# Kernel optimization log

Hardware: AMD Instinct MI355X
Metric: run time of the kernel (lower is better)

The kernel has to match this reference:

```python
import jax, jax.numpy as jnp
import numpy as np

B, S, D = 2, 2048, 1024
H = 16
HD = D // H


def setup_inputs() -> dict:
    key = jax.random.key(0)
    k = jax.random.split(key, 5)
    s = 0.02
    return {
        "x": jax.random.normal(k[0], (B, S, D), jnp.float32),
        "w_qkv": jax.random.normal(k[1], (3 * D, D), jnp.float32) * s,
        "b_qkv": jax.random.normal(k[2], (3 * D,), jnp.float32) * s,
        "w_out": jax.random.normal(k[3], (D, D), jnp.float32) * s,
        "b_out": jax.random.normal(k[4], (D,), jnp.float32) * s,
    }


def reference(x, w_qkv, b_qkv, w_out, b_out):
    b, s, d = x.shape
    h, hd = H, HD
    scale = hd ** -0.5
    # QKV projection: [B,S,3D] -> [3,B,H,S,hd]
    qkv = x @ w_qkv.T + b_qkv
    qkv = qkv.reshape(b, s, 3, h, hd).transpose(2, 0, 3, 1, 4)
    q, k, v = qkv[0], qkv[1], qkv[2]
    # Attention scores [B,H,S,S]
    scores = jnp.einsum("bhqd,bhkd->bhqk", q, k) * scale
    attn = jax.nn.softmax(scores, axis=-1)
    # Attend and merge heads
    attended = jnp.einsum("bhqk,bhkd->bqhd", attn, v).reshape(b, s, d)
    return attended @ w_out.T + b_out
```

## Files before the change

### kernel.cpp

```cpp
#include <hip/hip_runtime.h>
#include <hip/hip_bf16.h>

typedef __hip_bfloat16 bf16;
typedef __attribute__((ext_vector_type(8))) short short8;
typedef __attribute__((ext_vector_type(8))) __bf16 bf16x8;
typedef __attribute__((ext_vector_type(2))) float f32x2;
typedef __attribute__((ext_vector_type(4))) float f32x4;
typedef __attribute__((ext_vector_type(16))) float f32x16;
typedef __attribute__((ext_vector_type(4))) unsigned int u32x4;
typedef __attribute__((ext_vector_type(2))) unsigned int u32x2;

#define MFMA16(a, b, c)                                                        \
  __builtin_amdgcn_mfma_f32_16x16x32_bf16(__builtin_bit_cast(bf16x8, (a)),     \
                                          __builtin_bit_cast(bf16x8, (b)),     \
                                          (c), 0, 0, 0)
#define MFMA32(a, b, c)                                                        \
  __builtin_amdgcn_mfma_f32_32x32x16_bf16(__builtin_bit_cast(bf16x8, (a)),     \
                                          __builtin_bit_cast(bf16x8, (b)),     \
                                          (c), 0, 0, 0)

#define GLD16(gsrc, ldst)                                                      \
  __builtin_amdgcn_global_load_lds(                                            \
      (const __attribute__((address_space(1))) void*)(gsrc),                   \
      (__attribute__((address_space(3))) void*)(ldst), 16, 0, 0)

__device__ inline unsigned pk2(float lo, float hi) {
  unsigned r;
  asm("v_cvt_pk_bf16_f32 %0, %1, %2" : "=v"(r) : "v"(lo), "v"(hi));
  return r;
}
__device__ inline f32x2 pkfma(f32x2 s, f32x2 m, f32x2 a) {
  f32x2 r;
  asm("v_pk_fma_f32 %0, %1, %2, %3" : "=v"(r) : "v"(s), "v"(m), "v"(a));
  return r;
}
__device__ inline short f2bfs(float f) {
  return __builtin_bit_cast(short, __float2bfloat16(f));
}

template <typename T> __device__ inline short8 ld8bf(const T* p);
template <> __device__ inline short8 ld8bf<bf16>(const bf16* p) {
  return *(const short8*)p;
}
template <> __device__ inline short8 ld8bf<float>(const float* p) {
  f32x4 a = *(const f32x4*)p;
  f32x4 b = *(const f32x4*)(p + 4);
  u32x4 r;
  r[0] = pk2(a[0], a[1]);
  r[1] = pk2(a[2], a[3]);
  r[2] = pk2(b[0], b[1]);
  r[3] = pk2(b[2], b[3]);
  return __builtin_bit_cast(short8, r);
}

template <typename OT> __device__ inline void st1(OT* p, float v);
template <> __device__ inline void st1<bf16>(bf16* p, float v) {
  *p = __float2bfloat16(v);
}
template <> __device__ inline void st1<float>(float* p, float v) { *p = v; }

__device__ inline unsigned int funnel16(unsigned int hi, unsigned int lo) {
  return (unsigned int)(((((unsigned long long)hi) << 32) | lo) >> 16);
}
__device__ inline short8 rotl8(short8 v, int r) {
  u32x4 W = __builtin_bit_cast(u32x4, v);
  u32x4 T, U, F;
  int wr = r >> 1;
  T[0] = (wr & 1) ? W[1] : W[0];
  T[1] = (wr & 1) ? W[2] : W[1];
  T[2] = (wr & 1) ? W[3] : W[2];
  T[3] = (wr & 1) ? W[0] : W[3];
  U[0] = (wr & 2) ? T[2] : T[0];
  U[1] = (wr & 2) ? T[3] : T[1];
  U[2] = (wr & 2) ? T[0] : T[2];
  U[3] = (wr & 2) ? T[1] : T[3];
  F[0] = (r & 1) ? funnel16(U[1], U[0]) : U[0];
  F[1] = (r & 1) ? funnel16(U[2], U[1]) : U[1];
  F[2] = (r & 1) ? funnel16(U[3], U[2]) : U[2];
  F[3] = (r & 1) ? funnel16(U[0], U[3]) : U[3];
  return __builtin_bit_cast(short8, F);
}

__global__ __launch_bounds__(256) void cvt3(
    const float* __restrict__ s0, bf16* __restrict__ d0, int n0,
    const float* __restrict__ s1, bf16* __restrict__ d1, int n1,
    const float* __restrict__ s2, bf16* __restrict__ d2, int n2) {
  int i = (blockIdx.x * 256 + threadIdx.x) * 8;
  if (i < n0) {
    *(short8*)&d0[i] = ld8bf(s0 + i);
  } else if ((i -= n0) < n1) {
    *(short8*)&d1[i] = ld8bf(s1 + i);
  } else if ((i -= n1) < n2) {
    *(short8*)&d2[i] = ld8bf(s2 + i);
  }
}

template <int BN, typename OT>
__global__ __launch_bounds__(256, 2) void gemm_lds_bias(
    const bf16* __restrict__ A, const bf16* __restrict__ B,
    const float* __restrict__ bias, OT* __restrict__ C, int M, int N, int K) {
  __shared__ bf16 As[128][64];
  __shared__ bf16 Bs[BN][64];

  const int tid = threadIdx.x;
  const int w = tid >> 6, l = tid & 63;
  const int wr = w >> 1, wc = w & 1;
  const int m0 = blockIdx.y * 128, n0 = blockIdx.x * BN;
  const int JN = BN / 64;
  const int WCOL = BN / 2;

  f32x4 acc[4][2 * JN] = {};

  const int srow = l >> 3;
  const int scol = (l & 7) * 8;

  for (int kt = 0; kt < K; kt += 64) {
#pragma unroll
    for (int j = 0; j < 4; ++j) {
      int chunk = w * 4 + j;
      int row = chunk * 8 + srow;
      GLD16(A + (size_t)(m0 + row) * K + kt + scol, &As[0][0] + chunk * 512);
    }
#pragma unroll
    for (int j = 0; j < BN / 32; ++j) {
      int chunk = w * (BN / 32) + j;
      int row = chunk * 8 + srow;
      GLD16(B + (size_t)(n0 + row) * K + kt + scol, &Bs[0][0] + chunk * 512);
    }
    __syncthreads();

#pragma unroll
    for (int kk = 0; kk < 2; ++kk) {
      short8 af[4], bfv[2 * JN];
#pragma unroll
      for (int i = 0; i < 4; ++i)
        af[i] = *(const short8*)&As[wr * 64 + i * 16 + (l & 15)]
                                  [kk * 32 + (l >> 4) * 8];
#pragma unroll
      for (int jn = 0; jn < 2 * JN; ++jn)
        bfv[jn] = *(const short8*)&Bs[wc * WCOL + jn * 16 + (l & 15)]
                                    [kk * 32 + (l >> 4) * 8];
#pragma unroll
      for (int i = 0; i < 4; ++i)
#pragma unroll
        for (int jn = 0; jn < 2 * JN; ++jn)
          acc[i][jn] = MFMA16(af[i], bfv[jn], acc[i][jn]);
    }
    __syncthreads();
  }

#pragma unroll
  for (int i = 0; i < 4; ++i) {
    int rbase = m0 + wr * 64 + i * 16 + (l >> 4) * 4;
#pragma unroll
    for (int jn = 0; jn < 2 * JN; ++jn) {
      int col = n0 + wc * WCOL + jn * 16 + (l & 15);
      float bv = bias[col];
#pragma unroll
      for (int r = 0; r < 4; ++r)
        st1(&C[(size_t)(rbase + r) * N + col], acc[i][jn][r] + bv);
    }
  }
}

template <typename AT, typename OT>
__global__ __launch_bounds__(256, 2) void gemm_bt_bias(
    const AT* __restrict__ A, const float* __restrict__ B,
    const float* __restrict__ bias, OT* __restrict__ C, int M, int N, int K) {
  __shared__ bf16 As[128][64];
  __shared__ bf16 Bs[128][64];

  const int tid = threadIdx.x;
  const int w = tid >> 6, l = tid & 63;
  const int wr = w >> 1, wc = w & 1;
  const int m0 = blockIdx.y * 128, n0 = blockIdx.x * 128;

  f32x4 acc[4][4] = {};

  const int srow = tid >> 3;
  const int scol = (tid & 7) * 8;

  for (int kt = 0; kt < K; kt += 64) {
    short8 aReg[4], bReg[4];
#pragma unroll
    for (int p = 0; p < 4; ++p) {
      int row = p * 32 + srow;
      aReg[p] = ld8bf(A + (size_t)(m0 + row) * K + kt + scol);
      bReg[p] = ld8bf(B + (size_t)(n0 + row) * K + kt + scol);
    }
    __syncthreads();
#pragma unroll
    for (int p = 0; p < 4; ++p) {
      int row = p * 32 + srow;
      *(short8*)&As[row][scol] = aReg[p];
      *(short8*)&Bs[row][scol] = bReg[p];
    }
    __syncthreads();

#pragma unroll
    for (int kk = 0; kk < 2; ++kk) {
      short8 af[4], bfv[4];
#pragma unroll
      for (int i = 0; i < 4; ++i) {
        af[i]  = *(const short8*)&As[wr * 64 + i * 16 + (l & 15)]
                                   [kk * 32 + (l >> 4) * 8];
        bfv[i] = *(const short8*)&Bs[wc * 64 + i * 16 + (l & 15)]
                                   [kk * 32 + (l >> 4) * 8];
      }
#pragma unroll
      for (int i = 0; i < 4; ++i)
#pragma unroll
        for (int jn = 0; jn < 4; ++jn)
          acc[i][jn] = MFMA16(af[i], bfv[jn], acc[i][jn]);
    }
  }

#pragma unroll
  for (int i = 0; i < 4; ++i) {
    int rbase = m0 + wr * 64 + i * 16 + (l >> 4) * 4;
#pragma unroll
    for (int jn = 0; jn < 4; ++jn) {
      int col = n0 + wc * 64 + jn * 16 + (l & 15);
      float bv = bias[col];
#pragma unroll
      for (int r = 0; r < 4; ++r)
        st1(&C[(size_t)(rbase + r) * N + col], acc[i][jn][r] + bv);
    }
  }
}

__global__ __launch_bounds__(256, 2) void attn_fwd(
    const bf16* __restrict__ qkv, bf16* __restrict__ attended) {
  const int S = 2048, D3 = 3072, D = 1024;
  const int flat = blockIdx.y * 16 + blockIdx.x;
  const int n = (flat & 7) * 64 + (flat >> 3);
  const int qt = n & 15, bh = n >> 4;
  const int b = bh >> 4, h = bh & 15;
  const int tid = threadIdx.x, w = tid >> 6, l = tid & 63;
  const int lo5 = l & 31, hi = l >> 5;

  __shared__ bf16 Klds[128][72];
  __shared__ bf16 Vt[64][136];

  const int q0w = qt * 128 + w * 32;

  short8 qf[4];
  {
    size_t qrow = (size_t)(b * S + q0w + lo5) * D3 + h * 64;
#pragma unroll
    for (int ks = 0; ks < 4; ++ks)
      qf[ks] = *(const short8*)&qkv[qrow + ks * 16 + hi * 8];
  }

  const u32x4 onesw = {0x3F803F80u, 0x3F803F80u, 0x3F803F80u, 0x3F803F80u};
  const short8 ones = __builtin_bit_cast(short8, onesw);

  float m_raw = -1e30f;
  f32x16 o0 = {}, o1 = {}, oL = {};

  const float Cs = 0.125f * 1.44269504088896340736f;

  const int srow = tid >> 2;
  const int scq = tid & 3;
  const size_t gb0 = (size_t)(b * S + srow) * D3 + h * 64 + scq * 16;
  const size_t HSTEP = (size_t)64 * D3;

  short8 k0, k1, k2, k3, v0, v1, v2, v3;
  {
    const bf16* g = qkv + gb0;
    k0 = *(const short8*)&g[1024];
    k1 = *(const short8*)&g[1024 + 8];
    v0 = *(const short8*)&g[2048];
    v1 = *(const short8*)&g[2048 + 8];
    const bf16* g2 = g + HSTEP;
    k2 = *(const short8*)&g2[1024];
    k3 = *(const short8*)&g2[1024 + 8];
    v2 = *(const short8*)&g2[2048];
    v3 = *(const short8*)&g2[2048 + 8];
  }

#define PACKP(G, SV)                                                           \
  {                                                                            \
    _Pragma("unroll") for (int tq = 0; tq < 4; ++tq) {                         \
      po[G][tq][0] = pk2((SV)[4 * tq], (SV)[4 * tq + 1]);                      \
      po[G][tq][1] = pk2((SV)[4 * tq + 2], (SV)[4 * tq + 3]);                  \
    }                                                                          \
  }
#define EXPP(SV)                                                               \
  {                                                                            \
    _Pragma("unroll") for (int r2 = 0; r2 < 8; ++r2) {                         \
      f32x2 p;                                                                 \
      p[0] = (SV)[2 * r2];                                                     \
      p[1] = (SV)[2 * r2 + 1];                                                 \
      p = pkfma(p, csc, npc);                                                  \
      (SV)[2 * r2] = __builtin_amdgcn_exp2f(p[0]);                             \
      (SV)[2 * r2 + 1] = __builtin_amdgcn_exp2f(p[1]);                         \
    }                                                                          \
  }

  for (int t = 0; t < 16; ++t) {
    __syncthreads();
    *(short8*)&Klds[srow][scq * 16] = k0;
    *(short8*)&Klds[srow][scq * 16 + 8] = k1;
    *(short8*)&Klds[64 + srow][scq * 16] = k2;
    *(short8*)&Klds[64 + srow][scq * 16 + 8] = k3;
#pragma unroll
    for (int g = 0; g < 2; ++g) {
      int sI = scq * 2 + g;
      short8 ua = rotl8(g ? v1 : v0, sI);
      short8 ub = rotl8(g ? v3 : v2, sI);
#pragma unroll
      for (int j = 0; j < 8; ++j) {
        int jj = (j + sI) & 7;
        *(short*)&Vt[sI * 8 + jj][srow] = (short)ua[j];
        *(short*)&Vt[sI * 8 + jj][64 + srow] = (short)ub[j];
      }
    }
    __syncthreads();

    if (t + 1 < 16) {
      const bf16* g = qkv + gb0 + (size_t)(t + 1) * 2 * HSTEP;
      k0 = *(const short8*)&g[1024];
      k1 = *(const short8*)&g[1024 + 8];
      k2 = *(const short8*)&g[HSTEP + 1024];
      k3 = *(const short8*)&g[HSTEP + 1024 + 8];
    }

    f32x16 s0 = {}, s1 = {}, s2 = {}, s3 = {};
    __builtin_amdgcn_s_setprio(1);
#pragma unroll
    for (int ks = 0; ks < 4; ++ks) {
      short8 km0 = *(const short8*)&Klds[lo5][ks * 16 + hi * 8];
      short8 km1 = *(const short8*)&Klds[32 + lo5][ks * 16 + hi * 8];
      short8 km2 = *(const short8*)&Klds[64 + lo5][ks * 16 + hi * 8];
      short8 km3 = *(const short8*)&Klds[96 + lo5][ks * 16 + hi * 8];
      s0 = MFMA32(km0, qf[ks], s0);
      s1 = MFMA32(km1, qf[ks], s1);
      s2 = MFMA32(km2, qf[ks], s2);
      s3 = MFMA32(km3, qf[ks], s3);
    }
    __builtin_amdgcn_s_setprio(0);

    if (t + 1 < 16) {
      const bf16* g = qkv + gb0 + (size_t)(t + 1) * 2 * HSTEP;
      v0 = *(const short8*)&g[2048];
      v1 = *(const short8*)&g[2048 + 8];
      v2 = *(const short8*)&g[HSTEP + 2048];
      v3 = *(const short8*)&g[HSTEP + 2048 + 8];
    }

    f32x16 tm;
#pragma unroll
    for (int r = 0; r < 16; ++r)
      tm[r] = fmaxf(fmaxf(fmaxf(s0[r], s1[r]), s2[r]), s3[r]);
    float a0 = fmaxf(fmaxf(tm[0], tm[1]), tm[2]);
    float a1 = fmaxf(fmaxf(tm[3], tm[4]), tm[5]);
    float a2 = fmaxf(fmaxf(tm[6], tm[7]), tm[8]);
    float a3 = fmaxf(fmaxf(tm[9], tm[10]), tm[11]);
    float a4 = fmaxf(fmaxf(tm[12], tm[13]), tm[14]);
    float b0v = fmaxf(fmaxf(a0, a1), a2);
    float b1v = fmaxf(fmaxf(a3, a4), tm[15]);
    float mx = fmaxf(b0v, b1v);
    mx = fmaxf(mx, __shfl_xor(mx, 32));

    bool deferred = __all((mx - m_raw) * Cs <= 8.0f);
    if (!deferred) {
      float mn = fmaxf(m_raw, mx);
      float alpha = __builtin_amdgcn_exp2f((m_raw - mn) * Cs);
      m_raw = mn;
      o0 *= alpha;
      o1 *= alpha;
      oL *= alpha;
    }
    float pc = m_raw * Cs;
    f32x2 csc, npc;
    csc[0] = Cs; csc[1] = Cs;
    npc[0] = -pc; npc[1] = -pc;

    EXPP(s0) EXPP(s1) EXPP(s2) EXPP(s3)

    unsigned po[4][4][2];
    PACKP(0, s0) PACKP(1, s1) PACKP(2, s2) PACKP(3, s3)

    __builtin_amdgcn_s_setprio(1);
#pragma unroll
    for (int ks2 = 0; ks2 < 8; ++ks2) {
      const int g = ks2 >> 1, p = ks2 & 1;
      u32x2 ra = __builtin_amdgcn_permlane32_swap(po[g][2 * p][0],
                                                  po[g][2 * p + 1][0],
                                                  false, false);
      u32x2 rb = __builtin_amdgcn_permlane32_swap(po[g][2 * p][1],
                                                  po[g][2 * p + 1][1],
                                                  false, false);
      u32x4 fw;
      fw[0] = ra[0];
      fw[1] = rb[0];
      fw[2] = ra[1];
      fw[3] = rb[1];
      short8 pf = __builtin_bit_cast(short8, fw);
      short8 va0 = *(const short8*)&Vt[lo5][ks2 * 16 + hi * 8];
      short8 va1 = *(const short8*)&Vt[32 + lo5][ks2 * 16 + hi * 8];
      o0 = MFMA32(va0, pf, o0);
      o1 = MFMA32(va1, pf, o1);
      oL = MFMA32(ones, pf, oL);
    }
    __builtin_amdgcn_s_setprio(0);
  }

  float inv = 1.0f / oL[0];
  size_t orow = (size_t)(b * S + q0w + lo5) * D + h * 64;
#pragma unroll
  for (int t = 0; t < 4; ++t) {
    u32x2 w0, w1;
    w0[0] = pk2(o0[4 * t] * inv, o0[4 * t + 1] * inv);
    w0[1] = pk2(o0[4 * t + 2] * inv, o0[4 * t + 3] * inv);
    w1[0] = pk2(o1[4 * t] * inv, o1[4 * t + 1] * inv);
    w1[1] = pk2(o1[4 * t + 2] * inv, o1[4 * t + 3] * inv);
    *(u32x2*)&attended[orow + 8 * t + 4 * hi] = w0;
    *(u32x2*)&attended[orow + 32 + 8 * t + 4 * hi] = w1;
  }
}

extern "C" void kernel_launch(void* const* d_in, const int* in_sizes, int n_in,
                              void* d_out, int out_size, void* d_ws,
                              size_t ws_size, hipStream_t stream) {
  const float* x     = (const float*)d_in[0];
  const float* w_qkv = (const float*)d_in[1];
  const float* b_qkv = (const float*)d_in[2];
  const float* w_out = (const float*)d_in[3];
  const float* b_out = (const float*)d_in[4];
  float* out = (float*)d_out;

  const int BS = 4096;
  const int D = 1024, D3 = 3072;
  const int NX = BS * D, NWQ = D3 * D, NWO = D * D;

  bf16* qkv = (bf16*)d_ws;
  bf16* att = qkv + (size_t)BS * D3;

  const size_t NEED = ((size_t)BS * D3 + (size_t)BS * D + (size_t)D3 * D +
                       (size_t)D * D) * sizeof(bf16);

  if (ws_size >= NEED) {
    bf16* xb  = att;
    bf16* wqb = xb + (size_t)NX;
    bf16* wob = wqb + (size_t)NWQ;

    int ncvt = (NX + NWQ + NWO) / 8;
    cvt3<<<(ncvt + 255) / 256, 256, 0, stream>>>(x, xb, NX, w_qkv, wqb, NWQ,
                                                 w_out, wob, NWO);
    gemm_lds_bias<128, bf16><<<dim3(D3 / 128, BS / 128), 256, 0, stream>>>(
        xb, wqb, b_qkv, qkv, BS, D3, D);
    attn_fwd<<<dim3(16, 32), 256, 0, stream>>>(qkv, att);
    gemm_lds_bias<64, float><<<dim3(D / 64, BS / 128), 256, 0, stream>>>(
        att, wob, b_out, out, BS, D, D);
  } else {
    gemm_bt_bias<float, bf16><<<dim3(D3 / 128, BS / 128), 256, 0, stream>>>(
        x, w_qkv, b_qkv, qkv, BS, D3, D);
    attn_fwd<<<dim3(16, 32), 256, 0, stream>>>(qkv, att);
    gemm_bt_bias<bf16, float><<<dim3(D / 128, BS / 128), 256, 0, stream>>>(
        att, w_out, b_out, out, BS, D, D);
  }
}
```

Baseline: 120.5 us.

## Split attention KV range in two halves and merge partials in a combine kernel

The attention kernel gains a split mode: each query tile processes only half of the key/value sequence, doubling the grid to 1024 blocks. Each block writes unnormalized bf16 partial outputs plus its row sum and running max to a workspace buffer. A new combine_halves kernel then rescales the two halves with the log-sum-exp correction and writes the normalized result. The goal is more parallelism and better CU fill. The cost is an extra kernel launch, extra global traffic for the partials, and some rounding from storing the partials in bf16.

```diff
diff --git a/kernel.cpp b/kernel.cpp
--- a/kernel.cpp
+++ b/kernel.cpp
@@ -36,6 +36,12 @@
 }
 __device__ inline short f2bfs(float f) {
   return __builtin_bit_cast(short, __float2bfloat16(f));
+}
+__device__ inline f32x2 upk2(unsigned u) {
+  f32x2 r;
+  r[0] = __builtin_bit_cast(float, u << 16);
+  r[1] = __builtin_bit_cast(float, u & 0xFFFF0000u);
+  return r;
 }
 
 template <typename T> __device__ inline short8 ld8bf(const T* p);
@@ -229,12 +235,27 @@
   }
 }
 
+template <int SPLIT>
 __global__ __launch_bounds__(256, 2) void attn_fwd(
-    const bf16* __restrict__ qkv, bf16* __restrict__ attended) {
+    const bf16* __restrict__ qkv, bf16* __restrict__ attended,
+    unsigned* __restrict__ part) {
   const int S = 2048, D3 = 3072, D = 1024;
-  const int flat = blockIdx.y * 16 + blockIdx.x;
-  const int n = (flat & 7) * 64 + (flat >> 3);
-  const int qt = n & 15, bh = n >> 4;
+  int qt, bh, half, unit;
+  if (SPLIT) {
+    const int flat = blockIdx.y * 16 + blockIdx.x;
+    const int n = (flat & 7) * 128 + (flat >> 3);
+    half = n & 1;
+    unit = n >> 1;
+    qt = unit & 15;
+    bh = unit >> 4;
+  } else {
+    const int flat = blockIdx.y * 16 + blockIdx.x;
+    const int n = (flat & 7) * 64 + (flat >> 3);
+    qt = n & 15;
+    bh = n >> 4;
+    half = 0;
+    unit = 0;
+  }
   const int b = bh >> 4, h = bh & 15;
   const int tid = threadIdx.x, w = tid >> 6, l = tid & 63;
   const int lo5 = l & 31, hi = l >> 5;
@@ -243,6 +264,8 @@
   __shared__ bf16 Vt[64][136];
 
   const int q0w = qt * 128 + w * 32;
+  const int NT = SPLIT ? 8 : 16;
+  const int kvbase = SPLIT ? half * 1024 : 0;
 
   short8 qf[4];
   {
@@ -262,7 +285,7 @@
 
   const int srow = tid >> 2;
   const int scq = tid & 3;
-  const size_t gb0 = (size_t)(b * S + srow) * D3 + h * 64 + scq * 16;
+  const size_t gb0 = (size_t)(b * S + kvbase + srow) * D3 + h * 64 + scq * 16;
   const size_t HSTEP = (size_t)64 * D3;
 
   short8 k0, k1, k2, k3, v0, v1, v2, v3;
@@ -298,7 +321,7 @@
     }                                                                          \
   }
 
-  for (int t = 0; t < 16; ++t) {
+  for (int t = 0; t < NT; ++t) {
     __syncthreads();
     *(short8*)&Klds[srow][scq * 16] = k0;
     *(short8*)&Klds[srow][scq * 16 + 8] = k1;
@@ -318,7 +341,7 @@
     }
     __syncthreads();
 
-    if (t + 1 < 16) {
+    if (t + 1 < NT) {
       const bf16* g = qkv + gb0 + (size_t)(t + 1) * 2 * HSTEP;
       k0 = *(const short8*)&g[1024];
       k1 = *(const short8*)&g[1024 + 8];
@@ -341,7 +364,7 @@
     }
     __builtin_amdgcn_s_setprio(0);
 
-    if (t + 1 < 16) {
+    if (t + 1 < NT) {
       const bf16* g = qkv + gb0 + (size_t)(t + 1) * 2 * HSTEP;
       v0 = *(const short8*)&g[2048];
       v1 = *(const short8*)&g[2048 + 8];
@@ -407,15 +430,68 @@
     __builtin_amdgcn_s_setprio(0);
   }
 
-  float inv = 1.0f / oL[0];
+  if (SPLIT) {
+    unsigned* blob = part + ((size_t)(unit * 2 + half) * 256 + tid) * 18;
+#pragma unroll
+    for (int t = 0; t < 4; ++t) {
+      blob[2 * t]     = pk2(o0[4 * t], o0[4 * t + 1]);
+      blob[2 * t + 1] = pk2(o0[4 * t + 2], o0[4 * t + 3]);
+      blob[8 + 2 * t]     = pk2(o1[4 * t], o1[4 * t + 1]);
+      blob[8 + 2 * t + 1] = pk2(o1[4 * t + 2], o1[4 * t + 3]);
+    }
+    blob[16] = __builtin_bit_cast(unsigned, oL[0]);
+    blob[17] = __builtin_bit_cast(unsigned, m_raw);
+  } else {
+    float inv = 1.0f / oL[0];
+    size_t orow = (size_t)(b * S + q0w + lo5) * D + h * 64;
+#pragma unroll
+    for (int t = 0; t < 4; ++t) {
+      u32x2 w0, w1;
+      w0[0] = pk2(o0[4 * t] * inv, o0[4 * t + 1] * inv);
+      w0[1] = pk2(o0[4 * t + 2] * inv, o0[4 * t + 3] * inv);
+      w1[0] = pk2(o1[4 * t] * inv, o1[4 * t + 1] * inv);
+      w1[1] = pk2(o1[4 * t + 2] * inv, o1[4 * t + 3] * inv);
+      *(u32x2*)&attended[orow + 8 * t + 4 * hi] = w0;
+      *(u32x2*)&attended[orow + 32 + 8 * t + 4 * hi] = w1;
+    }
+  }
+}
+
+__global__ __launch_bounds__(256) void combine_halves(
+    const unsigned* __restrict__ part, bf16* __restrict__ attended) {
+  const int S = 2048, D = 1024;
+  const int unit = blockIdx.x;
+  const int qt = unit & 15, bh = unit >> 4;
+  const int b = bh >> 4, h = bh & 15;
+  const int tid = threadIdx.x, w = tid >> 6, l = tid & 63;
+  const int lo5 = l & 31, hi = l >> 5;
+  const float Cs = 0.125f * 1.44269504088896340736f;
+
+  const unsigned* bA = part + ((size_t)(unit * 2 + 0) * 256 + tid) * 18;
+  const unsigned* bB = part + ((size_t)(unit * 2 + 1) * 256 + tid) * 18;
+
+  float lA = __builtin_bit_cast(float, bA[16]);
+  float mA = __builtin_bit_cast(float, bA[17]);
+  float lB = __builtin_bit_cast(float, bB[16]);
+  float mB = __builtin_bit_cast(float, bB[17]);
+  float m = fmaxf(mA, mB);
+  float aA = __builtin_amdgcn_exp2f((mA - m) * Cs);
+  float aB = __builtin_amdgcn_exp2f((mB - m) * Cs);
+  float inv = 1.0f / (aA * lA + aB * lB);
+  float cA = aA * inv, cB = aB * inv;
+
+  const int q0w = qt * 128 + w * 32;
   size_t orow = (size_t)(b * S + q0w + lo5) * D + h * 64;
 #pragma unroll
   for (int t = 0; t < 4; ++t) {
     u32x2 w0, w1;
-    w0[0] = pk2(o0[4 * t] * inv, o0[4 * t + 1] * inv);
-    w0[1] = pk2(o0[4 * t + 2] * inv, o0[4 * t + 3] * inv);
-    w1[0] = pk2(o1[4 * t] * inv, o1[4 * t + 1] * inv);
-    w1[1] = pk2(o1[4 * t + 2] * inv, o1[4 * t + 3] * inv);
+#pragma unroll
+    for (int hf = 0; hf < 2; ++hf) {
+      f32x2 xa0 = upk2(bA[2 * t + hf]), xb0 = upk2(bB[2 * t + hf]);
+      f32x2 xa1 = upk2(bA[8 + 2 * t + hf]), xb1 = upk2(bB[8 + 2 * t + hf]);
+      w0[hf] = pk2(cA * xa0[0] + cB * xb0[0], cA * xa0[1] + cB * xb0[1]);
+      w1[hf] = pk2(cA * xa1[0] + cB * xb1[0], cA * xa1[1] + cB * xb1[1]);
+    }
     *(u32x2*)&attended[orow + 8 * t + 4 * hi] = w0;
     *(u32x2*)&attended[orow + 32 + 8 * t + 4 * hi] = w1;
   }
@@ -434,30 +510,53 @@
   const int BS = 4096;
   const int D = 1024, D3 = 3072;
   const int NX = BS * D, NWQ = D3 * D, NWO = D * D;
+  const int ncvt = (NX + NWQ + NWO) / 8;
 
   bf16* qkv = (bf16*)d_ws;
-  bf16* att = qkv + (size_t)BS * D3;
-
-  const size_t NEED = ((size_t)BS * D3 + (size_t)BS * D + (size_t)D3 * D +
-                       (size_t)D * D) * sizeof(bf16);
-
-  if (ws_size >= NEED) {
-    bf16* xb  = att;
+
+  const size_t PARTU32 = (size_t)512 * 2 * 256 * 18;
+  const size_t NEED2 = ((size_t)BS * D3 + (size_t)D * D + (size_t)BS * D) * 2 +
+                       ((size_t)NX + NWQ) * 2 > PARTU32 * 4
+                           ? ((size_t)BS * D3 + D * D + BS * D) * 2 +
+                                 ((size_t)NX + NWQ) * 2
+                           : ((size_t)BS * D3 + D * D + BS * D) * 2 +
+                                 PARTU32 * 4;
+  const size_t NEED1 = ((size_t)BS * D3 + (size_t)BS * D + (size_t)D3 * D +
+                        (size_t)D * D) * sizeof(bf16);
+
+  if (ws_size >= NEED2) {
+    bf16* wob = qkv + (size_t)BS * D3;
+    bf16* att = wob + (size_t)NWO;
+    bf16* xb  = att + (size_t)NX;
     bf16* wqb = xb + (size_t)NX;
-    bf16* wob = wqb + (size_t)NWQ;
-
-    int ncvt = (NX + NWQ + NWO) / 8;
+    unsigned* partials = (unsigned*)xb;
+
     cvt3<<<(ncvt + 255) / 256, 256, 0, stream>>>(x, xb, NX, w_qkv, wqb, NWQ,
                                                  w_out, wob, NWO);
     gemm_lds_bias<128, bf16><<<dim3(D3 / 128, BS / 128), 256, 0, stream>>>(
         xb, wqb, b_qkv, qkv, BS, D3, D);
-    attn_fwd<<<dim3(16, 32), 256, 0, stream>>>(qkv, att);
+    attn_fwd<1><<<dim3(16, 64), 256, 0, stream>>>(qkv, nullptr, partials);
+    combine_halves<<<512, 256, 0, stream>>>(partials, att);
+    gemm_lds_bias<64, float><<<dim3(D / 64, BS / 128), 256, 0, stream>>>(
+        att, wob, b_out, out, BS, D, D);
+  } else if (ws_size >= NEED1) {
+    bf16* att = qkv + (size_t)BS * D3;
+    bf16* xb  = att;
+    bf16* wqb = xb + (size_t)NX;
+    bf16* wob = wqb + (size_t)NWQ;
+
+    cvt3<<<(ncvt + 255) / 256, 256, 0, stream>>>(x, xb, NX, w_qkv, wqb, NWQ,
+                                                 w_out, wob, NWO);
+    gemm_lds_bias<128, bf16><<<dim3(D3 / 128, BS / 128), 256, 0, stream>>>(
+        xb, wqb, b_qkv, qkv, BS, D3, D);
+    attn_fwd<0><<<dim3(16, 32), 256, 0, stream>>>(qkv, att, nullptr);
     gemm_lds_bias<64, float><<<dim3(D / 64, BS / 128), 256, 0, stream>>>(
         att, wob, b_out, out, BS, D, D);
   } else {
+    bf16* att = qkv + (size_t)BS * D3;
     gemm_bt_bias<float, bf16><<<dim3(D3 / 128, BS / 128), 256, 0, stream>>>(
         x, w_qkv, b_qkv, qkv, BS, D3, D);
-    attn_fwd<<<dim3(16, 32), 256, 0, stream>>>(qkv, att);
+    attn_fwd<0><<<dim3(16, 32), 256, 0, stream>>>(qkv, att, nullptr);
     gemm_bt_bias<bf16, float><<<dim3(D / 128, BS / 128), 256, 0, stream>>>(
         att, w_out, b_out, out, BS, D, D);
   }
```

After: 128.9 us. 7.0% more time.
